# Kernel optimization log

Measured on AMD Instinct MI355X. Metric: run time of the kernel, lower is better.

## Reference

```python
import jax, jax.numpy as jnp
import numpy as np

NUM_FILTERS = 512
NUM_HEADS = 8
D_HEAD = NUM_FILTERS // NUM_HEADS


def setup_inputs() -> dict:
    key = jax.random.key(0)
    ks = jax.random.split(key, 11)
    B, W, H, F = 4, 48, 48, NUM_FILTERS
    s = 1.0 / np.sqrt(F)
    return {
        "query": jax.random.normal(ks[0], (B, W, H, F), jnp.float32),
        "value": jax.random.normal(ks[1], (B, W, H, F), jnp.float32),
        "keys": jax.random.normal(ks[2], (B, W, H, F), jnp.float32),
        "wq_w": jax.random.normal(ks[3], (F, F), jnp.float32) * s,
        "wq_b": jnp.zeros((F,), jnp.float32),
        "wk_w": jax.random.normal(ks[4], (F, F), jnp.float32) * s,
        "wk_b": jnp.zeros((F,), jnp.float32),
        "wv_w": jax.random.normal(ks[5], (F, F), jnp.float32) * s,
        "wv_b": jnp.zeros((F,), jnp.float32),
        "wo_w": jax.random.normal(ks[6], (F, F), jnp.float32) * s,
        "wo_b": jnp.zeros((F,), jnp.float32),
    }


def reference(query, value, keys, wq_w, wq_b, wk_w, wk_b, wv_w, wv_b, wo_w, wo_b):
    B, W, H, F = query.shape
    h, d = NUM_HEADS, D_HEAD
    # flatten spatial -> sequence, project, split heads: [B, h, S, d]
    def proj(x, w, b):
        x = x.reshape(B, -1, F) @ w + b
        return x.reshape(B, -1, h, d).transpose(0, 2, 1, 3)
    q = proj(query, wq_w, wq_b)
    k = proj(keys, wk_w, wk_b)
    v = proj(value, wv_w, wv_b)
    # scaled dot-product attention (mask=None path)
    logits = jnp.einsum('bhqd,bhkd->bhqk', q, k) / jnp.sqrt(jnp.asarray(d, q.dtype))
    attn = jax.nn.softmax(logits, axis=-1)            # [B, h, S, S]
    ctx = jnp.einsum('bhqk,bhkd->bhqd', attn, v)      # [B, h, S, d]
    ctx = ctx.transpose(0, 2, 1, 3).reshape(B, -1, F)  # [B, S, F]
    out = (ctx @ wo_w + wo_b).reshape(B, W, H, F)
    attn_weights = attn.reshape(B, h, W, H, -1)        # [B, h, W, H, S]
    return out, attn_weights
```

## Files before the change

### kernel.cpp

```cpp
#include <hip/hip_runtime.h>
#include <cstddef>

#define BB 4
#define SS 2304
#define FF 512
#define NH 8
#define DD 64
#define BSR (BB*SS)

typedef __attribute__((ext_vector_type(8))) short bf16x8;
typedef __attribute__((ext_vector_type(4))) float f32x4;
#define MFMA16(a,b,c) __builtin_amdgcn_mfma_f32_16x16x32_bf16((a),(b),(c),0,0,0)

__device__ __forceinline__ ushort f2bf_rne(float x) {
    uint u = __float_as_uint(x);
    uint r = u + 0x7fffu + ((u >> 16) & 1u);
    return (ushort)(r >> 16);
}
__device__ __forceinline__ float bfval(ushort h) {
    return __uint_as_float((uint)h << 16);
}
__device__ __forceinline__ uint cvt_pk_bf16(float a, float b) {
    uint r;
    asm("v_cvt_pk_bf16_f32 %0, %1, %2" : "=v"(r) : "v"(a), "v"(b));
    return r;
}
__device__ __forceinline__ float lo16val(uint p) { return __uint_as_float(p << 16); }
__device__ __forceinline__ float hi16val(uint p) { return __uint_as_float(p & 0xffff0000u); }

__global__ __launch_bounds__(256) void wtsplit_all(
    const float* __restrict__ w0, const float* __restrict__ w1,
    const float* __restrict__ w2, const float* __restrict__ w3,
    ushort* __restrict__ whi_all, ushort* __restrict__ wlo_all)
{
    __shared__ __align__(16) float tile[64][68];
    const int z = blockIdx.z;
    const float* w = (z == 0) ? w0 : (z == 1) ? w1 : (z == 2) ? w2 : w3;
    ushort* whi = whi_all + (size_t)z * FF * FF;
    ushort* wlo = wlo_all + (size_t)z * FF * FF;

    const int t  = threadIdx.x;
    const int kt = blockIdx.x;
    const int nt = blockIdx.y;
    {
        const int r  = t >> 2;
        const int cg = (t & 3) * 16;
        const float* src = w + (size_t)(kt * 64 + r) * FF + nt * 64 + cg;
        #pragma unroll
        for (int j = 0; j < 4; ++j)
            *(float4*)&tile[r][cg + 4 * j] = *(const float4*)(src + 4 * j);
    }
    __syncthreads();
    {
        const int n  = t >> 2;
        const int kg = (t & 3) * 16;
        uint H[8], L[8];
        #pragma unroll
        for (int j = 0; j < 8; ++j) {
            float x0 = tile[kg + 2 * j][n];
            float x1 = tile[kg + 2 * j + 1][n];
            uint hp = cvt_pk_bf16(x0, x1);
            H[j] = hp;
            L[j] = cvt_pk_bf16(x0 - lo16val(hp), x1 - hi16val(hp));
        }
        size_t off = (size_t)(nt * 64 + n) * FF + kt * 64 + kg;
        *(uint4*)(whi + off)     = make_uint4(H[0], H[1], H[2], H[3]);
        *(uint4*)(whi + off + 8) = make_uint4(H[4], H[5], H[6], H[7]);
        *(uint4*)(wlo + off)     = make_uint4(L[0], L[1], L[2], L[3]);
        *(uint4*)(wlo + off + 8) = make_uint4(L[4], L[5], L[6], L[7]);
    }
}

__global__ __launch_bounds__(256) void proj_qkv(
    const float* __restrict__ q_in, const float* __restrict__ k_in,
    const float* __restrict__ v_in, const ushort* __restrict__ whi_all,
    const ushort* __restrict__ wlo_all, const float* __restrict__ bq,
    const float* __restrict__ bk, const float* __restrict__ bv,
    ushort* __restrict__ qhi, ushort* __restrict__ qlo,
    ushort* __restrict__ khi, ushort* __restrict__ klo,
    ushort* __restrict__ vthi)
{
    __shared__ __align__(16) ushort TL[9216];

    const int z = blockIdx.z;
    const float* X = (z == 0) ? q_in : (z == 1) ? k_in : v_in;
    const ushort* wth = whi_all + (size_t)z * FF * FF;
    const ushort* wtl = wlo_all + (size_t)z * FF * FF;
    const float* bias = (z == 0) ? bq : (z == 1) ? bk : bv;

    const int t  = threadIdx.x, w = t >> 6, l = t & 63;
    const int ar = l & 15, kg = (l >> 4) * 8;
    const int i0 = blockIdx.x * 64, j0 = blockIdx.y * 128;
    const int arow = i0 + w * 16 + ar;

    f32x4 acc[8];
    #pragma unroll
    for (int nt = 0; nt < 8; ++nt) acc[nt] = (f32x4){0.f, 0.f, 0.f, 0.f};

    for (int kk = 0; kk < FF; kk += 32) {
        const float* xr = X + (size_t)arow * FF + kk + kg;
        float4 f0 = *(const float4*)xr;
        float4 f1 = *(const float4*)(xr + 4);
        union { uint u[4]; bf16x8 v; } ah, al;
        ah.u[0] = cvt_pk_bf16(f0.x, f0.y);
        ah.u[1] = cvt_pk_bf16(f0.z, f0.w);
        ah.u[2] = cvt_pk_bf16(f1.x, f1.y);
        ah.u[3] = cvt_pk_bf16(f1.z, f1.w);
        if (z < 2) {
            al.u[0] = cvt_pk_bf16(f0.x - lo16val(ah.u[0]), f0.y - hi16val(ah.u[0]));
            al.u[1] = cvt_pk_bf16(f0.z - lo16val(ah.u[1]), f0.w - hi16val(ah.u[1]));
            al.u[2] = cvt_pk_bf16(f1.x - lo16val(ah.u[2]), f1.y - hi16val(ah.u[2]));
            al.u[3] = cvt_pk_bf16(f1.z - lo16val(ah.u[3]), f1.w - hi16val(ah.u[3]));
        }
        #pragma unroll
        for (int nt = 0; nt < 8; ++nt) {
            const size_t wo = (size_t)(j0 + nt * 16 + ar) * FF + kk + kg;
            bf16x8 bh = *(const bf16x8*)(wth + wo);
            bf16x8 bl = *(const bf16x8*)(wtl + wo);
            acc[nt] = MFMA16(ah.v, bh, acc[nt]);
            acc[nt] = MFMA16(ah.v, bl, acc[nt]);
            if (z < 2) acc[nt] = MFMA16(al.v, bh, acc[nt]);
        }
    }

    const int bidx = i0 / SS;
    const int s0b  = i0 - bidx * SS;
    const int rowl = w * 16 + ((l >> 4) << 2);

    if (z == 2) {
        #pragma unroll
        for (int nt = 0; nt < 8; ++nt) {
            const float bb = bias[j0 + nt * 16 + ar];
            #pragma unroll
            for (int r = 0; r < 4; ++r)
                TL[(nt * 16 + ar) * 72 + rowl + r] = f2bf_rne(acc[nt][r] + bb);
        }
        __syncthreads();
        const int d = t >> 1, hf = t & 1;
        const ushort* src = &TL[d * 72 + hf * 32];
        const size_t o = (((size_t)bidx * NH + ((j0 + d) >> 6)) * DD + (d & 63)) * SS
                       + s0b + hf * 32;
        *(uint4*)(vthi + o)      = *(const uint4*)(src);
        *(uint4*)(vthi + o + 8)  = *(const uint4*)(src + 8);
        *(uint4*)(vthi + o + 16) = *(const uint4*)(src + 16);
        *(uint4*)(vthi + o + 24) = *(const uint4*)(src + 24);
    } else {
        ushort* ohi = (z == 0) ? qhi : khi;
        ushort* olo = (z == 0) ? qlo : klo;
        const int rowf = t >> 2, qd = t & 3;
        const int colg = j0 + qd * 32;
        const size_t o = (((size_t)bidx * NH + (colg >> 6)) * SS + s0b + rowf) * DD
                       + (colg & 63);
        #pragma unroll
        for (int nt = 0; nt < 8; ++nt) {
            const float bb = bias[j0 + nt * 16 + ar];
            #pragma unroll
            for (int r = 0; r < 4; ++r)
                TL[(rowl + r) * 136 + nt * 16 + ar] = f2bf_rne(acc[nt][r] + bb);
        }
        __syncthreads();
        {
            const ushort* src = &TL[rowf * 136 + qd * 32];
            *(uint4*)(ohi + o)      = *(const uint4*)(src);
            *(uint4*)(ohi + o + 8)  = *(const uint4*)(src + 8);
            *(uint4*)(ohi + o + 16) = *(const uint4*)(src + 16);
            *(uint4*)(ohi + o + 24) = *(const uint4*)(src + 24);
        }
        __syncthreads();
        #pragma unroll
        for (int nt = 0; nt < 8; ++nt) {
            const float bb = bias[j0 + nt * 16 + ar];
            #pragma unroll
            for (int r = 0; r < 4; ++r) {
                const float val = acc[nt][r] + bb;
                const ushort hv = f2bf_rne(val);
                TL[(rowl + r) * 136 + nt * 16 + ar] = f2bf_rne(val - bfval(hv));
            }
        }
        __syncthreads();
        {
            const ushort* src = &TL[rowf * 136 + qd * 32];
            *(uint4*)(olo + o)      = *(const uint4*)(src);
            *(uint4*)(olo + o + 8)  = *(const uint4*)(src + 8);
            *(uint4*)(olo + o + 16) = *(const uint4*)(src + 16);
            *(uint4*)(olo + o + 24) = *(const uint4*)(src + 24);
        }
    }
}

__global__ __launch_bounds__(256) void proj_out(
    const float* __restrict__ X, const ushort* __restrict__ wth,
    const ushort* __restrict__ wtl, const float* __restrict__ bias,
    float* __restrict__ outf)
{
    const int t  = threadIdx.x, w = t >> 6, l = t & 63;
    const int ar = l & 15, kg = (l >> 4) * 8;
    const int i0 = blockIdx.x * 64, j0 = blockIdx.y * 128;
    const int arow = i0 + w * 16 + ar;

    f32x4 acc[8];
    #pragma unroll
    for (int nt = 0; nt < 8; ++nt) acc[nt] = (f32x4){0.f, 0.f, 0.f, 0.f};

    for (int kk = 0; kk < FF; kk += 32) {
        const float* xr = X + (size_t)arow * FF + kk + kg;
        float4 f0 = *(const float4*)xr;
        float4 f1 = *(const float4*)(xr + 4);
        union { uint u[4]; bf16x8 v; } ah;
        ah.u[0] = cvt_pk_bf16(f0.x, f0.y);
        ah.u[1] = cvt_pk_bf16(f0.z, f0.w);
        ah.u[2] = cvt_pk_bf16(f1.x, f1.y);
        ah.u[3] = cvt_pk_bf16(f1.z, f1.w);
        #pragma unroll
        for (int nt = 0; nt < 8; ++nt) {
            const size_t wo = (size_t)(j0 + nt * 16 + ar) * FF + kk + kg;
            bf16x8 bh = *(const bf16x8*)(wth + wo);
            bf16x8 bl = *(const bf16x8*)(wtl + wo);
            acc[nt] = MFMA16(ah.v, bh, acc[nt]);
            acc[nt] = MFMA16(ah.v, bl, acc[nt]);
        }
    }

    #pragma unroll
    for (int nt = 0; nt < 8; ++nt) {
        const int col = j0 + nt * 16 + ar;
        const float bb = bias[col];
        #pragma unroll
        for (int r = 0; r < 4; ++r) {
            const int rowl = w * 16 + (l >> 4) * 4 + r;
            outf[(size_t)(i0 + rowl) * FF + col] = acc[nt][r] + bb;
        }
    }
}

__global__ __launch_bounds__(512, 4) void fattn_kernel(
    const ushort* __restrict__ qhi, const ushort* __restrict__ qlo,
    const ushort* __restrict__ khi, const ushort* __restrict__ klo,
    const ushort* __restrict__ vthi,
    float* __restrict__ attn_out, float* __restrict__ ctx)
{
    __shared__ __align__(16) unsigned char smem[67584];
    ushort* KH0 = (ushort*)smem;
    ushort* KH1 = KH0 + 4096;
    ushort* KL0 = KH1 + 4096;
    ushort* KL1 = KL0 + 4096;
    ushort* VH0 = KL1 + 4096;
    ushort* VH1 = VH0 + 4096;
    float*  PT  = (float*)(VH1 + 4096);
    float*  redS = PT;

    const int t = threadIdx.x, w = t >> 6, l = t & 63;
    const int ar = l & 15, kgi = l >> 4;
    const int kg = kgi * 8;
    const int qs = w & 3, kh = w >> 2;

    const int xcd = blockIdx.x & 7;
    const int pos = blockIdx.x >> 3;
    const int bh  = xcd * 4 + (pos / 36);
    const int qt  = pos % 36;
    const int q0  = qt * 64;
    const int b   = bh >> 3, h = bh & 7;
    const size_t base = (size_t)bh * SS * DD;
    const float SC = 0.125f * 1.44269504f;

    const size_t qo = base + (size_t)(q0 + qs * 16 + ar) * DD + kg;
    const bf16x8 qh0 = *(const bf16x8*)(qhi + qo);
    const bf16x8 qh1 = *(const bf16x8*)(qhi + qo + 32);
    const bf16x8 ql0 = *(const bf16x8*)(qlo + qo);
    const bf16x8 ql1 = *(const bf16x8*)(qlo + qo + 32);

    const int srow = t >> 3, sc8 = t & 7;
    const int sidx = srow * 64 + ((sc8 ^ (srow & 7)) << 3);
    const ushort* khsrc = khi + base + srow * 64 + sc8 * 8;
    const ushort* klsrc = klo + base + srow * 64 + sc8 * 8;
    const ushort* vhsrc = vthi + ((size_t)bh * DD + srow) * SS + sc8 * 8;

    const int sw  = ar & 7;
    const int i00 = kh * 2048 + ar * 64;
    const int i01 = i00 + 1024;
    const int s00 = (kgi ^ sw) << 3;
    const int s01 = ((4 | kgi) ^ sw) << 3;
    const int svw = ((kh * 4 + kgi) ^ sw) << 3;

    float s_[4] = {0.f, 0.f, 0.f, 0.f};
    {
        uint4 rk = *(const uint4*)khsrc;
        *(uint4*)&KH0[sidx] = rk;
        __syncthreads();
        for (int kt = 0; kt < 36; ++kt) {
            if (kt < 35) rk = *(const uint4*)(khsrc + (size_t)(kt + 1) * 4096);
            const ushort* KC = (kt & 1) ? KH1 : KH0;
            bf16x8 b00 = *(const bf16x8*)&KC[i00 + s00];
            bf16x8 b01 = *(const bf16x8*)&KC[i00 + s01];
            bf16x8 b10 = *(const bf16x8*)&KC[i01 + s00];
            bf16x8 b11 = *(const bf16x8*)&KC[i01 + s01];
            f32x4 a0 = {0.f,0.f,0.f,0.f}, a1 = {0.f,0.f,0.f,0.f};
            __builtin_amdgcn_s_setprio(1);
            a0 = MFMA16(qh0, b00, a0); a1 = MFMA16(qh0, b10, a1);
            a0 = MFMA16(qh1, b01, a0); a1 = MFMA16(qh1, b11, a1);
            __builtin_amdgcn_s_setprio(0);
            #pragma unroll
            for (int r = 0; r < 4; ++r)
                s_[r] += exp2f(a0[r] * SC) + exp2f(a1[r] * SC);
            if (kt < 35) {
                ushort* KN = (kt & 1) ? KH0 : KH1;
                *(uint4*)&KN[sidx] = rk;
            }
            __syncthreads();
        }
    }
    #pragma unroll
    for (int off = 1; off <= 8; off <<= 1) {
        #pragma unroll
        for (int r = 0; r < 4; ++r) s_[r] += __shfl_xor(s_[r], off);
    }
    if (ar == 0) {
        #pragma unroll
        for (int r = 0; r < 4; ++r)
            redS[kh * 64 + qs * 16 + kgi * 4 + r] = s_[r];
    }
    __syncthreads();
    float linv[4];
    #pragma unroll
    for (int r = 0; r < 4; ++r) {
        const int idx = qs * 16 + kgi * 4 + r;
        linv[r] = -__log2f(redS[idx] + redS[64 + idx]);
    }

    float* PTw = PT + w * 576;
    float* asto = attn_out + ((size_t)bh * SS + q0 + qs * 16 + (l >> 2)) * SS
                + kh * 32 + (l & 3) * 8;

    f32x4 acc[4];
    #pragma unroll
    for (int nt = 0; nt < 4; ++nt) acc[nt] = (f32x4){0.f, 0.f, 0.f, 0.f};

    {
        uint4 a = *(const uint4*)khsrc;
        uint4 bq = *(const uint4*)klsrc;
        uint4 c = *(const uint4*)vhsrc;
        *(uint4*)&KH0[sidx] = a;
        *(uint4*)&KL0[sidx] = bq;
        *(uint4*)&VH0[sidx] = c;
    }
    __syncthreads();

    for (int kt = 0; kt < 36; ++kt) {
        uint4 rkh, rkl, rvh;
        if (kt < 35) {
            rkh = *(const uint4*)(khsrc + (size_t)(kt + 1) * 4096);
            rkl = *(const uint4*)(klsrc + (size_t)(kt + 1) * 4096);
            rvh = *(const uint4*)(vhsrc + (size_t)(kt + 1) * 64);
        }
        const ushort* KHc = (kt & 1) ? KH1 : KH0;
        const ushort* KLc = (kt & 1) ? KL1 : KL0;
        const ushort* VHc = (kt & 1) ? VH1 : VH0;

        bf16x8 bh00 = *(const bf16x8*)&KHc[i00 + s00];
        bf16x8 bh01 = *(const bf16x8*)&KHc[i00 + s01];
        bf16x8 bl00 = *(const bf16x8*)&KLc[i00 + s00];
        bf16x8 bl01 = *(const bf16x8*)&KLc[i00 + s01];
        bf16x8 bh10 = *(const bf16x8*)&KHc[i01 + s00];
        bf16x8 bh11 = *(const bf16x8*)&KHc[i01 + s01];
        bf16x8 bl10 = *(const bf16x8*)&KLc[i01 + s00];
        bf16x8 bl11 = *(const bf16x8*)&KLc[i01 + s01];
        f32x4 a0 = {0.f,0.f,0.f,0.f}, a1 = {0.f,0.f,0.f,0.f};
        __builtin_amdgcn_s_setprio(1);
        a0 = MFMA16(qh0, bh00, a0); a1 = MFMA16(qh0, bh10, a1);
        a0 = MFMA16(qh0, bl00, a0); a1 = MFMA16(qh0, bl10, a1);
        a0 = MFMA16(ql0, bh00, a0); a1 = MFMA16(ql0, bh10, a1);
        a0 = MFMA16(qh1, bh01, a0); a1 = MFMA16(qh1, bh11, a1);
        a0 = MFMA16(qh1, bl01, a0); a1 = MFMA16(qh1, bl11, a1);
        a0 = MFMA16(ql1, bh01, a0); a1 = MFMA16(ql1, bh11, a1);
        __builtin_amdgcn_s_setprio(0);

        #pragma unroll
        for (int r = 0; r < 4; ++r) {
            const int row = kgi * 4 + r;
            float p0 = exp2f(fmaf(a0[r], SC, linv[r]));
            float p1 = exp2f(fmaf(a1[r], SC, linv[r]));
            PTw[row * 36 + ar]      = p0;
            PTw[row * 36 + 16 + ar] = p1;
        }

        {
            const float* psr = PTw + (l >> 2) * 36 + (l & 3) * 8;
            f32x4 sv0 = *(const f32x4*)psr;
            f32x4 sv1 = *(const f32x4*)(psr + 4);
            f32x4* dst = (f32x4*)(asto + (size_t)kt * 64);
            __builtin_nontemporal_store(sv0, dst);
            __builtin_nontemporal_store(sv1, dst + 1);
        }

        {
            const float* par = PTw + ar * 36 + kg;
            f32x4 pf0 = *(const f32x4*)par;
            f32x4 pf1 = *(const f32x4*)(par + 4);
            union { uint u[4]; bf16x8 v; } pah, pal;
            pah.u[0] = cvt_pk_bf16(pf0[0], pf0[1]);
            pah.u[1] = cvt_pk_bf16(pf0[2], pf0[3]);
            pah.u[2] = cvt_pk_bf16(pf1[0], pf1[1]);
            pah.u[3] = cvt_pk_bf16(pf1[2], pf1[3]);
            pal.u[0] = cvt_pk_bf16(pf0[0] - lo16val(pah.u[0]), pf0[1] - hi16val(pah.u[0]));
            pal.u[1] = cvt_pk_bf16(pf0[2] - lo16val(pah.u[1]), pf0[3] - hi16val(pah.u[1]));
            pal.u[2] = cvt_pk_bf16(pf1[0] - lo16val(pah.u[2]), pf1[1] - hi16val(pah.u[2]));
            pal.u[3] = cvt_pk_bf16(pf1[2] - lo16val(pah.u[3]), pf1[3] - hi16val(pah.u[3]));
            __builtin_amdgcn_s_setprio(1);
            #pragma unroll
            for (int nt = 0; nt < 4; ++nt) {
                const int vfi = (nt * 16 + ar) * 64 + svw;
                bf16x8 vh = *(const bf16x8*)&VHc[vfi];
                acc[nt] = MFMA16(pah.v, vh, acc[nt]);
                acc[nt] = MFMA16(pal.v, vh, acc[nt]);
            }
            __builtin_amdgcn_s_setprio(0);
        }

        if (kt < 35) {
            ushort* KHN = (kt & 1) ? KH0 : KH1;
            ushort* KLN = (kt & 1) ? KL0 : KL1;
            ushort* VHN = (kt & 1) ? VH0 : VH1;
            *(uint4*)&KHN[sidx] = rkh;
            *(uint4*)&KLN[sidx] = rkl;
            *(uint4*)&VHN[sidx] = rvh;
        }
        __syncthreads();
    }

    float* SCR = (float*)smem;
    #pragma unroll
    for (int nt = 0; nt < 4; ++nt) {
        #pragma unroll
        for (int r = 0; r < 4; ++r)
            SCR[w * 1088 + (kgi * 4 + r) * 68 + nt * 16 + ar] = acc[nt][r];
    }
    __syncthreads();
    {
        const int rrow = t >> 3;
        const int dg   = (t & 7) * 8;
        const int rqs  = rrow >> 4, rl = rrow & 15;
        const float* s0p = SCR + rqs * 1088 + rl * 68 + dg;
        const float* s1p = s0p + 4 * 1088;
        f32x4 o0, o1;
        #pragma unroll
        for (int j = 0; j < 4; ++j) o0[j] = s0p[j] + s1p[j];
        #pragma unroll
        for (int j = 0; j < 4; ++j) o1[j] = s0p[4 + j] + s1p[4 + j];
        float* cdst = ctx + ((size_t)b * SS + q0 + rrow) * FF + h * DD + dg;
        *(f32x4*)cdst = o0;
        *(f32x4*)(cdst + 4) = o1;
    }
}

extern "C" void kernel_launch(void* const* d_in, const int* in_sizes, int n_in,
                              void* d_out, int out_size, void* d_ws, size_t ws_size,
                              hipStream_t stream) {
    (void)in_sizes; (void)n_in; (void)out_size; (void)ws_size;
    const float* query = (const float*)d_in[0];
    const float* value = (const float*)d_in[1];
    const float* keys  = (const float*)d_in[2];
    const float* wq_w  = (const float*)d_in[3];
    const float* wq_b  = (const float*)d_in[4];
    const float* wk_w  = (const float*)d_in[5];
    const float* wk_b  = (const float*)d_in[6];
    const float* wv_w  = (const float*)d_in[7];
    const float* wv_b  = (const float*)d_in[8];
    const float* wo_w  = (const float*)d_in[9];
    const float* wo_b  = (const float*)d_in[10];

    float* out  = (float*)d_out;
    float* attn = out + (size_t)BB * SS * FF;

    const size_t NQ = (size_t)BB * NH * SS * DD;
    ushort* qhi    = (ushort*)d_ws;
    ushort* qlo    = qhi + NQ;
    ushort* khi    = qlo + NQ;
    ushort* klo    = khi + NQ;
    ushort* vthi   = klo + NQ;
    float*  vstage = (float*)(vthi + NQ);
    ushort* wthi   = (ushort*)(vstage + NQ);
    ushort* wtlo   = wthi + (size_t)4 * FF * FF;

    dim3 gwt(FF / 64, FF / 64, 4);
    dim3 gqkv(BSR / 64, FF / 128, 3);
    dim3 gproj(BSR / 64, FF / 128);

    wtsplit_all<<<gwt, 256, 0, stream>>>(wq_w, wk_w, wv_w, wo_w, wthi, wtlo);
    proj_qkv<<<gqkv, 256, 0, stream>>>(query, keys, value, wthi, wtlo,
                                       wq_b, wk_b, wv_b,
                                       qhi, qlo, khi, klo, vthi);

    fattn_kernel<<<36 * 32, 512, 0, stream>>>(qhi, qlo, khi, klo, vthi,
                                              attn, vstage);

    proj_out<<<gproj, 256, 0, stream>>>(vstage, wthi + (size_t)3 * FF * FF,
                                        wtlo + (size_t)3 * FF * FF, wo_b, out);
}
```

Before: 603.4 us.

## Load K fragments directly from global memory instead of staging through LDS

K-hi and K-lo tiles are no longer copied into double-buffered shared memory. Each wave now reads its MFMA B fragments straight from global memory, which removes the K staging stores and the barriers in the row-sum pass. Shared memory per block roughly halves, which may allow more blocks per CU. The cost is that each K tile is re-read from global memory/L2 by waves that previously shared one LDS copy, so global load latency is exposed without software prefetch.

```diff
diff --git a/kernel.cpp b/kernel.cpp
--- a/kernel.cpp
+++ b/kernel.cpp
@@ -239,12 +239,8 @@
     const ushort* __restrict__ vthi,
     float* __restrict__ attn_out, float* __restrict__ ctx)
 {
-    __shared__ __align__(16) unsigned char smem[67584];
-    ushort* KH0 = (ushort*)smem;
-    ushort* KH1 = KH0 + 4096;
-    ushort* KL0 = KH1 + 4096;
-    ushort* KL1 = KL0 + 4096;
-    ushort* VH0 = KL1 + 4096;
+    __shared__ __align__(16) unsigned char smem[34816];
+    ushort* VH0 = (ushort*)smem;
     ushort* VH1 = VH0 + 4096;
     float*  PT  = (float*)(VH1 + 4096);
     float*  redS = PT;
@@ -269,45 +265,31 @@
     const bf16x8 ql0 = *(const bf16x8*)(qlo + qo);
     const bf16x8 ql1 = *(const bf16x8*)(qlo + qo + 32);
 
+    const ushort* khp = khi + base + (size_t)(kh * 32 + ar) * DD;
+    const ushort* klp = klo + base + (size_t)(kh * 32 + ar) * DD;
+
     const int srow = t >> 3, sc8 = t & 7;
     const int sidx = srow * 64 + ((sc8 ^ (srow & 7)) << 3);
-    const ushort* khsrc = khi + base + srow * 64 + sc8 * 8;
-    const ushort* klsrc = klo + base + srow * 64 + sc8 * 8;
     const ushort* vhsrc = vthi + ((size_t)bh * DD + srow) * SS + sc8 * 8;
 
     const int sw  = ar & 7;
-    const int i00 = kh * 2048 + ar * 64;
-    const int i01 = i00 + 1024;
-    const int s00 = (kgi ^ sw) << 3;
-    const int s01 = ((4 | kgi) ^ sw) << 3;
     const int svw = ((kh * 4 + kgi) ^ sw) << 3;
 
     float s_[4] = {0.f, 0.f, 0.f, 0.f};
-    {
-        uint4 rk = *(const uint4*)khsrc;
-        *(uint4*)&KH0[sidx] = rk;
-        __syncthreads();
-        for (int kt = 0; kt < 36; ++kt) {
-            if (kt < 35) rk = *(const uint4*)(khsrc + (size_t)(kt + 1) * 4096);
-            const ushort* KC = (kt & 1) ? KH1 : KH0;
-            bf16x8 b00 = *(const bf16x8*)&KC[i00 + s00];
-            bf16x8 b01 = *(const bf16x8*)&KC[i00 + s01];
-            bf16x8 b10 = *(const bf16x8*)&KC[i01 + s00];
-            bf16x8 b11 = *(const bf16x8*)&KC[i01 + s01];
-            f32x4 a0 = {0.f,0.f,0.f,0.f}, a1 = {0.f,0.f,0.f,0.f};
-            __builtin_amdgcn_s_setprio(1);
-            a0 = MFMA16(qh0, b00, a0); a1 = MFMA16(qh0, b10, a1);
-            a0 = MFMA16(qh1, b01, a0); a1 = MFMA16(qh1, b11, a1);
-            __builtin_amdgcn_s_setprio(0);
-            #pragma unroll
-            for (int r = 0; r < 4; ++r)
-                s_[r] += exp2f(a0[r] * SC) + exp2f(a1[r] * SC);
-            if (kt < 35) {
-                ushort* KN = (kt & 1) ? KH0 : KH1;
-                *(uint4*)&KN[sidx] = rk;
-            }
-            __syncthreads();
-        }
+    for (int kt = 0; kt < 36; ++kt) {
+        const ushort* kp = khp + (size_t)kt * 4096;
+        bf16x8 b00 = *(const bf16x8*)(kp + kg);
+        bf16x8 b01 = *(const bf16x8*)(kp + 32 + kg);
+        bf16x8 b10 = *(const bf16x8*)(kp + 1024 + kg);
+        bf16x8 b11 = *(const bf16x8*)(kp + 1024 + 32 + kg);
+        f32x4 a0 = {0.f,0.f,0.f,0.f}, a1 = {0.f,0.f,0.f,0.f};
+        __builtin_amdgcn_s_setprio(1);
+        a0 = MFMA16(qh0, b00, a0); a1 = MFMA16(qh0, b10, a1);
+        a0 = MFMA16(qh1, b01, a0); a1 = MFMA16(qh1, b11, a1);
+        __builtin_amdgcn_s_setprio(0);
+        #pragma unroll
+        for (int r = 0; r < 4; ++r)
+            s_[r] += exp2f(a0[r] * SC) + exp2f(a1[r] * SC);
     }
     #pragma unroll
     for (int off = 1; off <= 8; off <<= 1) {
@@ -336,34 +318,26 @@
     for (int nt = 0; nt < 4; ++nt) acc[nt] = (f32x4){0.f, 0.f, 0.f, 0.f};
 
     {
-        uint4 a = *(const uint4*)khsrc;
-        uint4 bq = *(const uint4*)klsrc;
         uint4 c = *(const uint4*)vhsrc;
-        *(uint4*)&KH0[sidx] = a;
-        *(uint4*)&KL0[sidx] = bq;
         *(uint4*)&VH0[sidx] = c;
     }
     __syncthreads();
 
     for (int kt = 0; kt < 36; ++kt) {
-        uint4 rkh, rkl, rvh;
-        if (kt < 35) {
-            rkh = *(const uint4*)(khsrc + (size_t)(kt + 1) * 4096);
-            rkl = *(const uint4*)(klsrc + (size_t)(kt + 1) * 4096);
-            rvh = *(const uint4*)(vhsrc + (size_t)(kt + 1) * 64);
-        }
-        const ushort* KHc = (kt & 1) ? KH1 : KH0;
-        const ushort* KLc = (kt & 1) ? KL1 : KL0;
+        uint4 rvh;
+        if (kt < 35) rvh = *(const uint4*)(vhsrc + (size_t)(kt + 1) * 64);
         const ushort* VHc = (kt & 1) ? VH1 : VH0;
 
-        bf16x8 bh00 = *(const bf16x8*)&KHc[i00 + s00];
-        bf16x8 bh01 = *(const bf16x8*)&KHc[i00 + s01];
-        bf16x8 bl00 = *(const bf16x8*)&KLc[i00 + s00];
-        bf16x8 bl01 = *(const bf16x8*)&KLc[i00 + s01];
-        bf16x8 bh10 = *(const bf16x8*)&KHc[i01 + s00];
-        bf16x8 bh11 = *(const bf16x8*)&KHc[i01 + s01];
-        bf16x8 bl10 = *(const bf16x8*)&KLc[i01 + s00];
-        bf16x8 bl11 = *(const bf16x8*)&KLc[i01 + s01];
+        const ushort* kp = khp + (size_t)kt * 4096;
+        const ushort* lp = klp + (size_t)kt * 4096;
+        bf16x8 bh00 = *(const bf16x8*)(kp + kg);
+        bf16x8 bh01 = *(const bf16x8*)(kp + 32 + kg);
+        bf16x8 bh10 = *(const bf16x8*)(kp + 1024 + kg);
+        bf16x8 bh11 = *(const bf16x8*)(kp + 1024 + 32 + kg);
+        bf16x8 bl00 = *(const bf16x8*)(lp + kg);
+        bf16x8 bl01 = *(const bf16x8*)(lp + 32 + kg);
+        bf16x8 bl10 = *(const bf16x8*)(lp + 1024 + kg);
+        bf16x8 bl11 = *(const bf16x8*)(lp + 1024 + 32 + kg);
         f32x4 a0 = {0.f,0.f,0.f,0.f}, a1 = {0.f,0.f,0.f,0.f};
         __builtin_amdgcn_s_setprio(1);
         a0 = MFMA16(qh0, bh00, a0); a1 = MFMA16(qh0, bh10, a1);
@@ -417,11 +391,7 @@
         }
 
         if (kt < 35) {
-            ushort* KHN = (kt & 1) ? KH0 : KH1;
-            ushort* KLN = (kt & 1) ? KL0 : KL1;
             ushort* VHN = (kt & 1) ? VH0 : VH1;
-            *(uint4*)&KHN[sidx] = rkh;
-            *(uint4*)&KLN[sidx] = rkl;
             *(uint4*)&VHN[sidx] = rvh;
         }
         __syncthreads();
```

After: 895.8 us. 48.5% more time.
